# Performance work log

Measured on AMD Instinct MI355X. Metric: run time of the kernel, lower is better.

Reference implementation:

```python
import jax, jax.numpy as jnp
import numpy as np
import math

D_MODEL = 1024
NUM_HEADS = 16
HEAD_DIM = D_MODEL // NUM_HEADS
BATCH = 2
SEQ = 2048
THETA = 10000.0


def _rope_tables(seq_len, head_dim, theta=THETA):
    inv_freq = 1.0 / theta ** (jnp.arange(0, head_dim, 2, dtype=jnp.float32) / head_dim)
    pos = jnp.arange(seq_len, dtype=jnp.float32)
    freqs = jnp.outer(pos, inv_freq)                 # [S, hd/2]
    emb = jnp.concatenate([freqs, freqs], axis=-1)   # [S, hd]
    return jnp.cos(emb), jnp.sin(emb)


def _rotate_half(x):
    x1, x2 = jnp.split(x, 2, axis=-1)
    return jnp.concatenate([-x2, x1], axis=-1)


def setup_inputs() -> dict:
    key = jax.random.key(0)
    k1, k2, k3 = jax.random.split(key, 3)
    x = jax.random.normal(k1, (BATCH, SEQ, D_MODEL), dtype=jnp.float32)
    # causal mask: 1 where attend allowed, 0 where masked
    mask = jnp.tril(jnp.ones((SEQ, SEQ), dtype=jnp.int32))[None, None]
    w_qkv = jax.random.normal(k2, (D_MODEL, 3 * D_MODEL), dtype=jnp.float32) / math.sqrt(D_MODEL)
    w_out = jax.random.normal(k3, (D_MODEL, D_MODEL), dtype=jnp.float32) / math.sqrt(D_MODEL)
    return {"x": x, "mask": mask, "w_qkv": w_qkv, "w_out": w_out}


def reference(x, mask, w_qkv, w_out):
    B, S, _ = x.shape
    qkv = x @ w_qkv                                          # [B,S,3*D]
    qkv = qkv.reshape(B, S, 3, NUM_HEADS, HEAD_DIM)
    qkv = jnp.transpose(qkv, (2, 0, 3, 1, 4))                # [3,B,H,S,hd]
    q, k, v = qkv[0], qkv[1], qkv[2]
    cos, sin = _rope_tables(S, HEAD_DIM)                     # [S,hd]
    cos = cos[None, None]; sin = sin[None, None]
    q = q * cos + _rotate_half(q) * sin
    k = k * cos + _rotate_half(k) * sin
    scores = jnp.einsum('bhqd,bhkd->bhqk', q, k) / math.sqrt(HEAD_DIM)
    scores = jnp.where(mask == 0, -jnp.inf, scores)
    attn = jax.nn.softmax(scores, axis=-1)                   # dropout p=0 (eval)
    out = jnp.einsum('bhqk,bhkd->bhqd', attn, v)             # [B,H,S,hd]
    out = jnp.transpose(out, (0, 2, 1, 3)).reshape(B, S, D_MODEL)
    return out @ w_out
```

## Files before the change

kernel.cpp:

```cpp
#include <hip/hip_runtime.h>

typedef __bf16 bf16;
typedef __bf16 bf16x4 __attribute__((ext_vector_type(4)));
typedef __bf16 bf16x8 __attribute__((ext_vector_type(8)));
typedef short s16x4 __attribute__((ext_vector_type(4)));
typedef float f32x4 __attribute__((ext_vector_type(4)));

constexpr int BATCH = 2;
constexpr int SEQ   = 2048;
constexpr int DMODEL= 1024;
constexpr int NH    = 16;
constexpr int HD    = 64;
constexpr int M_ROWS= BATCH * SEQ;
constexpr int N_QKV = 3 * DMODEL;

__device__ __forceinline__ void gl_lds16(const bf16* g, bf16* l) {
  __builtin_amdgcn_global_load_lds(
      (const __attribute__((address_space(1))) unsigned int*)g,
      (__attribute__((address_space(3))) unsigned int*)l, 16, 0, 0);
}

__device__ __forceinline__ f32x4 mfma_16x16x16_bf16(bf16x4 a, bf16x4 b,
                                                    f32x4 c) {
#if defined(__HIP_DEVICE_COMPILE__)
  union { bf16x4 h; s16x4 s; } ua{a}, ub{b};
  return __builtin_amdgcn_mfma_f32_16x16x16bf16_1k(ua.s, ub.s, c, 0, 0, 0);
#else
  return c;
#endif
}

__global__ __launch_bounds__(256) void prep_kernel(
    const float* __restrict__ x, const float* __restrict__ w_qkv,
    const float* __restrict__ w_out, bf16* __restrict__ xb,
    bf16* __restrict__ WqkvT, bf16* __restrict__ WoutT) {
  const int bx = blockIdx.x, t = threadIdx.x;
  if (bx < 2048) {
    const int i = (bx * 256 + t) * 8;
    float4 f0 = *(const float4*)&x[i];
    float4 f1 = *(const float4*)&x[i + 4];
    bf16x8 v;
    v[0] = (bf16)f0.x; v[1] = (bf16)f0.y; v[2] = (bf16)f0.z; v[3] = (bf16)f0.w;
    v[4] = (bf16)f1.x; v[5] = (bf16)f1.y; v[6] = (bf16)f1.z; v[7] = (bf16)f1.w;
    *(bf16x8*)&xb[i] = v;
    return;
  }
  __shared__ float tile[32][33];
  const float* src;
  bf16* dst;
  int R, C, c0, r0;
  if (bx < 5120) {
    const int idx = bx - 2048;
    src = w_qkv; dst = WqkvT; R = DMODEL; C = N_QKV;
    c0 = (idx % 96) * 32; r0 = (idx / 96) * 32;
  } else {
    const int idx = bx - 5120;
    src = w_out; dst = WoutT; R = DMODEL; C = DMODEL;
    c0 = (idx & 31) * 32; r0 = (idx >> 5) * 32;
  }
  const int tx = t & 31, ty = t >> 5;
#pragma unroll
  for (int i = 0; i < 4; i++)
    tile[ty + 8 * i][tx] = src[(size_t)(r0 + ty + 8 * i) * C + c0 + tx];
  __syncthreads();
#pragma unroll
  for (int i = 0; i < 4; i++)
    dst[(size_t)(c0 + ty + 8 * i) * R + r0 + tx] = (bf16)tile[tx][ty + 8 * i];
}

#define GEMM_BODY(A, BT, K)                                                    \
  __shared__ bf16 smem[8448];                                                  \
  bf16* As = smem;                                                             \
  bf16* Bs = smem + 4096;                                                      \
  const int t = threadIdx.x;                                                   \
  const int m0 = blockIdx.y * 128;                                             \
  const int n0 = blockIdx.x * 128;                                             \
  const int w = t >> 6, lane = t & 63, g = lane >> 4, li = lane & 15;          \
  const int r0w = (w & 1) * 64, c0w = (w >> 1) * 64;                           \
  f32x4 acc[4][4] = {};                                                        \
  for (int k0 = 0; k0 < (K); k0 += 32) {                                       \
    __syncthreads();                                                           \
    _Pragma("unroll") for (int c = 0; c < 2; c++) {                            \
      const int idx = (w * 2 + c) * 64 + lane;                                 \
      const int row = idx >> 2, col = (idx & 3) * 8;                           \
      gl_lds16(&(A)[(size_t)(m0 + row) * (K) + k0 + col],                      \
               &As[(w * 2 + c) * 512]);                                        \
      gl_lds16(&(BT)[(size_t)(n0 + row) * (K) + k0 + col],                     \
               &Bs[(w * 2 + c) * 512]);                                        \
    }                                                                          \
    __syncthreads();                                                           \
    bf16x8 a[4], b[4];                                                         \
    _Pragma("unroll") for (int mt = 0; mt < 4; mt++)                           \
        a[mt] = *(const bf16x8*)&As[(r0w + mt * 16 + li) * 32 + g * 8];        \
    _Pragma("unroll") for (int nt = 0; nt < 4; nt++)                           \
        b[nt] = *(const bf16x8*)&Bs[(c0w + nt * 16 + li) * 32 + g * 8];        \
    _Pragma("unroll") for (int mt = 0; mt < 4; mt++)                           \
        _Pragma("unroll") for (int nt = 0; nt < 4; nt++)                       \
            acc[mt][nt] = __builtin_amdgcn_mfma_f32_16x16x32_bf16(             \
                a[mt], b[nt], acc[mt][nt], 0, 0, 0);                           \
  }

__global__ __launch_bounds__(256) void gemm_out64(
    const bf16* __restrict__ A, const bf16* __restrict__ BT,
    float* __restrict__ C, int M, int N, int K) {
  __shared__ bf16 As[64 * 32];
  __shared__ bf16 Bs[128 * 32];
  const int t = threadIdx.x;
  const int m0 = blockIdx.y * 64;
  const int n0 = blockIdx.x * 128;
  const int w = t >> 6, lane = t & 63, g = lane >> 4, li = lane & 15;
  const int r0w = (w & 1) * 32, c0w = (w >> 1) * 64;
  f32x4 acc[2][4] = {};
  for (int k0 = 0; k0 < K; k0 += 32) {
    __syncthreads();
    {
      const int idx = w * 64 + lane;
      const int row = idx >> 2, col = (idx & 3) * 8;
      gl_lds16(&A[(size_t)(m0 + row) * K + k0 + col], &As[w * 512]);
    }
#pragma unroll
    for (int c = 0; c < 2; c++) {
      const int idx = (w * 2 + c) * 64 + lane;
      const int row = idx >> 2, col = (idx & 3) * 8;
      gl_lds16(&BT[(size_t)(n0 + row) * K + k0 + col], &Bs[(w * 2 + c) * 512]);
    }
    __syncthreads();
    bf16x8 a[2], b[4];
#pragma unroll
    for (int mt = 0; mt < 2; mt++)
      a[mt] = *(const bf16x8*)&As[(r0w + mt * 16 + li) * 32 + g * 8];
#pragma unroll
    for (int nt = 0; nt < 4; nt++)
      b[nt] = *(const bf16x8*)&Bs[(c0w + nt * 16 + li) * 32 + g * 8];
#pragma unroll
    for (int mt = 0; mt < 2; mt++)
#pragma unroll
      for (int nt = 0; nt < 4; nt++)
        acc[mt][nt] = __builtin_amdgcn_mfma_f32_16x16x32_bf16(
            a[mt], b[nt], acc[mt][nt], 0, 0, 0);
  }
#pragma unroll
  for (int mt = 0; mt < 2; mt++)
#pragma unroll
    for (int nt = 0; nt < 4; nt++)
#pragma unroll
      for (int r = 0; r < 4; r++) {
        const int m = m0 + r0w + mt * 16 + g * 4 + r;
        const int n = n0 + c0w + nt * 16 + li;
        C[(size_t)m * N + n] = acc[mt][nt][r];
      }
}

__global__ __launch_bounds__(256) void gemm_qkv_rope(
    const bf16* __restrict__ A, const bf16* __restrict__ BT,
    bf16* __restrict__ Qb, bf16* __restrict__ Kb, bf16* __restrict__ Vt) {
  constexpr int K = DMODEL;
  GEMM_BODY(A, BT, K)

  const int region = n0 >> 10;
  const int b = m0 >> 11;
  const int h = ((n0 + c0w) >> 6) & 15;
  const size_t bh = (size_t)(b * NH + h);

  if (region < 2) {
    bf16* dst = region == 0 ? Qb : Kb;
    const float outsc = region == 0 ? 0.125f * 1.44269504f : 1.f;
    const float L = 13.287712379549449f;
    const float if0 = exp2f(-(float)(2 * li) / 64.f * L);
    const float if1 = exp2f(-(float)(2 * (li + 16)) / 64.f * L);
    bf16* lw = smem + w * 2112;
#pragma unroll
    for (int pass = 0; pass < 2; pass++) {
      __syncthreads();
#pragma unroll
      for (int mtl = 0; mtl < 2; mtl++) {
        const int mt = pass * 2 + mtl;
#pragma unroll
        for (int r = 0; r < 4; r++) {
          const int s = (m0 + r0w + mt * 16 + g * 4 + r) & (SEQ - 1);
          float cs[2], sn[2];
          __sincosf((float)s * if0, &sn[0], &cs[0]);
          __sincosf((float)s * if1, &sn[1], &cs[1]);
#pragma unroll
          for (int nt = 0; nt < 4; nt++) {
            const int par = nt & 1;
            const float a = acc[mt][nt][r];
            const float ap = acc[mt][nt ^ 2][r];
            const float v = (nt < 2) ? a * cs[par] - ap * sn[par]
                                     : a * cs[par] + ap * sn[par];
            lw[(mtl * 16 + g * 4 + r) * 66 + nt * 16 + li] =
                (bf16)(v * outsc);
          }
        }
      }
      __syncthreads();
      const int rowl = lane >> 1, dh = (lane & 1) * 32;
      const int s = (m0 + r0w + pass * 32 + rowl) & (SEQ - 1);
      bf16* gdst = &dst[(bh * SEQ + s) * HD + dh];
      const bf16* lsrc = &lw[rowl * 66 + dh];
#pragma unroll
      for (int c = 0; c < 4; c++)
        *(bf16x8*)&gdst[c * 8] = *(const bf16x8*)&lsrc[c * 8];
    }
  } else {
#pragma unroll
    for (int mt = 0; mt < 4; mt++)
#pragma unroll
      for (int nt = 0; nt < 4; nt++) {
        const int s = (m0 + r0w + mt * 16 + g * 4) & (SEQ - 1);
        const int d = nt * 16 + li;
        bf16x4 v;
#pragma unroll
        for (int r = 0; r < 4; r++) v[r] = (bf16)acc[mt][nt][r];
        *(bf16x4*)&Vt[(bh * HD + d) * SEQ + s] = v;
      }
  }
}

__global__ __launch_bounds__(256, 4) void flash_attn8(
    const bf16* __restrict__ Q, const bf16* __restrict__ Kb,
    const bf16* __restrict__ Vt, bf16* __restrict__ Oout) {
  const int bx = blockIdx.x;
  const int qt = 31 - (bx >> 5);
  const int bh = bx & 31;
  const int q0 = qt * 64;
  const int t = threadIdx.x, w = t >> 6, lane = t & 63, g = lane >> 4,
            li = lane & 15;

  __shared__ bf16 Ks[2][4096];
  __shared__ bf16 Vs[2][4096];

  const bf16* Qh = Q  + (size_t)bh * SEQ * HD;
  const bf16* Kh = Kb + (size_t)bh * SEQ * HD;
  const bf16* Vh = Vt + (size_t)bh * HD * SEQ;

  const int qw = q0 + w * 16;

  bf16x8 qf[2];
#pragma unroll
  for (int ks = 0; ks < 2; ks++)
    qf[ks] = *(const bf16x8*)&Qh[(size_t)(qw + li) * HD + ks * 32 + g * 8];

  f32x4 o[4] = {};
  f32x4 o4  = {};
  bf16x4 ones;
#pragma unroll
  for (int r = 0; r < 4; r++) ones[r] = (bf16)1.f;

  const int p0 = w * 128 + lane, p1 = p0 + 64;
  const int sr0 = p0 >> 3, sc0 = ((p0 & 7) ^ (sr0 & 7)) * 8;
  const int sr1 = p1 >> 3, sc1 = ((p1 & 7) ^ (sr1 & 7)) * 8;
  const int lo0 = w * 1024, lo1 = w * 1024 + 512;

  const int jend = q0 + 64;

  gl_lds16(&Kh[(size_t)sr0 * HD + sc0], &Ks[0][lo0]);
  gl_lds16(&Kh[(size_t)sr1 * HD + sc1], &Ks[0][lo1]);
  gl_lds16(&Vh[(size_t)sr0 * SEQ + sc0], &Vs[0][lo0]);
  gl_lds16(&Vh[(size_t)sr1 * SEQ + sc1], &Vs[0][lo1]);
  __syncthreads();

  for (int j0 = 0; j0 < jend; j0 += 64) {
    const int cur = (j0 >> 6) & 1, nxt = cur ^ 1;
    if (j0 + 64 < jend) {
      const int jn = j0 + 64;
      gl_lds16(&Kh[(size_t)(jn + sr0) * HD + sc0], &Ks[nxt][lo0]);
      gl_lds16(&Kh[(size_t)(jn + sr1) * HD + sc1], &Ks[nxt][lo1]);
      gl_lds16(&Vh[(size_t)sr0 * SEQ + jn + sc0], &Vs[nxt][lo0]);
      gl_lds16(&Vh[(size_t)sr1 * SEQ + jn + sc1], &Vs[nxt][lo1]);
    }

    if (j0 <= qw + 15) {
      const bool masked = (j0 + 63 > qw);
      const int ntlim = min(4, ((qw + 15 - j0) >> 4) + 1);

      f32x4 sacc[4] = {};
#pragma unroll
      for (int ks = 0; ks < 2; ks++)
#pragma unroll
        for (int nt = 0; nt < 4; nt++) {
          if (nt >= ntlim) continue;
          const int rK = nt * 16 + li;
          const int pK = rK * 8 + ((ks * 4 + g) ^ (li & 7));
          bf16x8 kf = *(const bf16x8*)&Ks[cur][pK * 8];
          sacc[nt] = __builtin_amdgcn_mfma_f32_16x16x32_bf16(kf, qf[ks],
                                                             sacc[nt], 0, 0, 0);
        }

      bf16x4 pf[4];
#pragma unroll
      for (int nt = 0; nt < 4; nt++) {
        if (nt >= ntlim) continue;
#pragma unroll
        for (int r = 0; r < 4; r++) {
          float v = sacc[nt][r];
          if (masked) {
            const int kk = j0 + nt * 16 + g * 4 + r;
            v = (kk <= qw + li) ? v : -1e30f;
          }
          pf[nt][r] = (bf16)exp2f(v);
        }
      }

#pragma unroll
      for (int nt = 0; nt < 4; nt++) {
        if (nt >= ntlim) continue;
        o4 = mfma_16x16x16_bf16(ones, pf[nt], o4);
#pragma unroll
        for (int dt = 0; dt < 4; dt++) {
          const int rV = dt * 16 + li;
          const int cg = nt * 2 + (g >> 1);
          const int pV = rV * 8 + (cg ^ (rV & 7));
          bf16x4 vfrag = *(const bf16x4*)&Vs[cur][pV * 8 + (g & 1) * 4];
          o[dt] = mfma_16x16x16_bf16(vfrag, pf[nt], o[dt]);
        }
      }
    }
    __syncthreads();
  }

  const float inv_l = 1.f / o4[0];

  const int b = bh >> 4, h = bh & 15;
  const int s = qw + li;
#pragma unroll
  for (int dt = 0; dt < 4; dt++) {
    bf16x4 ov;
#pragma unroll
    for (int r = 0; r < 4; r++) ov[r] = (bf16)(o[dt][r] * inv_l);
    *(bf16x4*)&Oout[((size_t)(b * SEQ + s)) * DMODEL + h * 64 + dt * 16 +
                    g * 4] = ov;
  }
}

extern "C" void kernel_launch(void* const* d_in, const int* in_sizes, int n_in,
                              void* d_out, int out_size, void* d_ws,
                              size_t ws_size, hipStream_t stream) {
  const float* x     = (const float*)d_in[0];
  const float* w_qkv = (const float*)d_in[2];
  const float* w_out = (const float*)d_in[3];
  float* out = (float*)d_out;

  char* ws = (char*)d_ws;
  bf16* WqkvT = (bf16*)(ws);
  bf16* WoutT = (bf16*)(ws + 6291456);
  bf16* xb    = (bf16*)(ws + 8388608);
  bf16* Qb    = (bf16*)(ws + 16777216);
  bf16* Kbuf  = (bf16*)(ws + 25165824);
  bf16* Vt    = (bf16*)(ws + 33554432);
  bf16* attn  = (bf16*)(ws + 41943040);

  prep_kernel<<<dim3(6144), 256, 0, stream>>>(x, w_qkv, w_out, xb, WqkvT,
                                              WoutT);
  gemm_qkv_rope<<<dim3(N_QKV / 128, M_ROWS / 128), 256, 0, stream>>>(
      xb, WqkvT, Qb, Kbuf, Vt);
  flash_attn8<<<dim3(1024), 256, 0, stream>>>(Qb, Kbuf, Vt, attn);
  gemm_out64<<<dim3(DMODEL / 128, M_ROWS / 64), 256, 0, stream>>>(
      attn, WoutT, out, M_ROWS, DMODEL, DMODEL);
}
```

Before: 207.0 us.

## Triple-buffer K/V tiles in flash attention with explicit vmcnt waits and priority

Switches the attention kernel's K/V shared-memory staging from double to triple buffering, so each loop iteration prefetches two tiles ahead. The full __syncthreads is replaced by explicit s_waitcnt vmcnt counts plus raw s_barrier and sched_barrier, which lets one tile's loads stay in flight across the barrier. MFMA sections are wrapped in s_setprio raises. The costs are 48KB of LDS per block and launch bounds lowered from 4 to 3 blocks per CU, which may reduce occupancy.

```diff
diff --git a/kernel.cpp b/kernel.cpp
--- a/kernel.cpp
+++ b/kernel.cpp
@@ -217,7 +217,7 @@
   }
 }
 
-__global__ __launch_bounds__(256, 4) void flash_attn8(
+__global__ __launch_bounds__(256, 3) void flash_attn9(
     const bf16* __restrict__ Q, const bf16* __restrict__ Kb,
     const bf16* __restrict__ Vt, bf16* __restrict__ Oout) {
   const int bx = blockIdx.x;
@@ -227,8 +227,8 @@
   const int t = threadIdx.x, w = t >> 6, lane = t & 63, g = lane >> 4,
             li = lane & 15;
 
-  __shared__ bf16 Ks[2][4096];
-  __shared__ bf16 Vs[2][4096];
+  __shared__ bf16 Ks[3][4096];
+  __shared__ bf16 Vs[3][4096];
 
   const bf16* Qh = Q  + (size_t)bh * SEQ * HD;
   const bf16* Kh = Kb + (size_t)bh * SEQ * HD;
@@ -240,6 +240,7 @@
 #pragma unroll
   for (int ks = 0; ks < 2; ks++)
     qf[ks] = *(const bf16x8*)&Qh[(size_t)(qw + li) * HD + ks * 32 + g * 8];
+  asm volatile("s_waitcnt vmcnt(0)" ::: "memory");
 
   f32x4 o[4] = {};
   f32x4 o4  = {};
@@ -252,29 +253,39 @@
   const int sr1 = p1 >> 3, sc1 = ((p1 & 7) ^ (sr1 & 7)) * 8;
   const int lo0 = w * 1024, lo1 = w * 1024 + 512;
 
-  const int jend = q0 + 64;
-
-  gl_lds16(&Kh[(size_t)sr0 * HD + sc0], &Ks[0][lo0]);
-  gl_lds16(&Kh[(size_t)sr1 * HD + sc1], &Ks[0][lo1]);
-  gl_lds16(&Vh[(size_t)sr0 * SEQ + sc0], &Vs[0][lo0]);
-  gl_lds16(&Vh[(size_t)sr1 * SEQ + sc1], &Vs[0][lo1]);
-  __syncthreads();
-
-  for (int j0 = 0; j0 < jend; j0 += 64) {
-    const int cur = (j0 >> 6) & 1, nxt = cur ^ 1;
-    if (j0 + 64 < jend) {
-      const int jn = j0 + 64;
-      gl_lds16(&Kh[(size_t)(jn + sr0) * HD + sc0], &Ks[nxt][lo0]);
-      gl_lds16(&Kh[(size_t)(jn + sr1) * HD + sc1], &Ks[nxt][lo1]);
-      gl_lds16(&Vh[(size_t)sr0 * SEQ + jn + sc0], &Vs[nxt][lo0]);
-      gl_lds16(&Vh[(size_t)sr1 * SEQ + jn + sc1], &Vs[nxt][lo1]);
-    }
+  const int ntiles = qt + 1;
+
+#define STAGE_T(ti, buf)                                                 \
+  {                                                                      \
+    const int jn = (ti) * 64;                                            \
+    gl_lds16(&Kh[(size_t)(jn + sr0) * HD + sc0], &Ks[buf][lo0]);         \
+    gl_lds16(&Kh[(size_t)(jn + sr1) * HD + sc1], &Ks[buf][lo1]);         \
+    gl_lds16(&Vh[(size_t)sr0 * SEQ + jn + sc0], &Vs[buf][lo0]);          \
+    gl_lds16(&Vh[(size_t)sr1 * SEQ + jn + sc1], &Vs[buf][lo1]);          \
+  }
+
+  STAGE_T(0, 0);
+  if (ntiles > 1) {
+    STAGE_T(1, 1);
+    asm volatile("s_waitcnt vmcnt(4)" ::: "memory");
+  } else {
+    asm volatile("s_waitcnt vmcnt(0)" ::: "memory");
+  }
+  __builtin_amdgcn_s_barrier();
+  __builtin_amdgcn_sched_barrier(0);
+
+  int cur = 0, stb = 2;
+  for (int ti = 0; ti < ntiles; ++ti) {
+    const int j0 = ti * 64;
+    const bool more2 = (ti + 2 < ntiles);
+    if (more2) STAGE_T(ti + 2, stb);
 
     if (j0 <= qw + 15) {
       const bool masked = (j0 + 63 > qw);
       const int ntlim = min(4, ((qw + 15 - j0) >> 4) + 1);
 
       f32x4 sacc[4] = {};
+      __builtin_amdgcn_s_setprio(1);
 #pragma unroll
       for (int ks = 0; ks < 2; ks++)
 #pragma unroll
@@ -286,6 +297,7 @@
           sacc[nt] = __builtin_amdgcn_mfma_f32_16x16x32_bf16(kf, qf[ks],
                                                              sacc[nt], 0, 0, 0);
         }
+      __builtin_amdgcn_s_setprio(0);
 
       bf16x4 pf[4];
 #pragma unroll
@@ -302,6 +314,7 @@
         }
       }
 
+      __builtin_amdgcn_s_setprio(1);
 #pragma unroll
       for (int nt = 0; nt < 4; nt++) {
         if (nt >= ntlim) continue;
@@ -315,9 +328,21 @@
           o[dt] = mfma_16x16x16_bf16(vfrag, pf[nt], o[dt]);
         }
       }
+      __builtin_amdgcn_s_setprio(0);
     }
-    __syncthreads();
-  }
+
+    __builtin_amdgcn_sched_barrier(0);
+    if (more2)
+      asm volatile("s_waitcnt vmcnt(4)" ::: "memory");
+    else
+      asm volatile("s_waitcnt vmcnt(0)" ::: "memory");
+    __builtin_amdgcn_s_barrier();
+    __builtin_amdgcn_sched_barrier(0);
+
+    cur = (cur == 2) ? 0 : cur + 1;
+    stb = (stb == 2) ? 0 : stb + 1;
+  }
+#undef STAGE_T
 
   const float inv_l = 1.f / o4[0];
 
@@ -354,7 +379,7 @@
                                               WoutT);
   gemm_qkv_rope<<<dim3(N_QKV / 128, M_ROWS / 128), 256, 0, stream>>>(
       xb, WqkvT, Qb, Kbuf, Vt);
-  flash_attn8<<<dim3(1024), 256, 0, stream>>>(Qb, Kbuf, Vt, attn);
+  flash_attn9<<<dim3(1024), 256, 0, stream>>>(Qb, Kbuf, Vt, attn);
   gemm_out64<<<dim3(DMODEL / 128, M_ROWS / 64), 256, 0, stream>>>(
       attn, WoutT, out, M_ROWS, DMODEL, DMODEL);
 }
```

Result: no change. 209.2 us (+1.1%).

## Split long causal query tiles across key chunks with atomic fp32 accumulation

Applied to the files above, without the earlier changes.

Query tiles beyond the first 512 rows are split into up to four key-range chunks of 8 tiles each. A lookup table orders the 2560 blocks so the heaviest work is scheduled first. Partial unnormalized outputs and row sums are combined with fp32 atomicAdd into a zeroed workspace, and a new attn_norm kernel divides by the sum and writes bf16. The aim is to cut the long-tail imbalance of causal attention and give the GPU more parallel work. The cost is many global atomics, an extra zeroing pass folded into prep, and one extra kernel launch.

```diff
diff --git a/kernel.cpp b/kernel.cpp
--- a/kernel.cpp
+++ b/kernel.cpp
@@ -33,7 +33,8 @@
 __global__ __launch_bounds__(256) void prep_kernel(
     const float* __restrict__ x, const float* __restrict__ w_qkv,
     const float* __restrict__ w_out, bf16* __restrict__ xb,
-    bf16* __restrict__ WqkvT, bf16* __restrict__ WoutT) {
+    bf16* __restrict__ WqkvT, bf16* __restrict__ WoutT,
+    float* __restrict__ zbase) {
   const int bx = blockIdx.x, t = threadIdx.x;
   if (bx < 2048) {
     const int i = (bx * 256 + t) * 8;
@@ -43,6 +44,13 @@
     v[0] = (bf16)f0.x; v[1] = (bf16)f0.y; v[2] = (bf16)f0.z; v[3] = (bf16)f0.w;
     v[4] = (bf16)f1.x; v[5] = (bf16)f1.y; v[6] = (bf16)f1.z; v[7] = (bf16)f1.w;
     *(bf16x8*)&xb[i] = v;
+    return;
+  }
+  if (bx >= 6144) {
+    const size_t base = ((size_t)(bx - 6144) * 256 + t) * 16;
+    const float4 z = {0.f, 0.f, 0.f, 0.f};
+#pragma unroll
+    for (int i = 0; i < 4; i++) *(float4*)&zbase[base + i * 4] = z;
     return;
   }
   __shared__ float tile[32][33];
@@ -217,13 +225,28 @@
   }
 }
 
-__global__ __launch_bounds__(256, 4) void flash_attn8(
+__device__ const unsigned char CHUNK_TAB[80] = {
+    124, 125, 126, 127,
+    120, 121, 122, 116, 117, 118, 112, 113, 114, 108, 109, 110,
+    104, 105, 106, 100, 101, 102, 96,  97,  98,  92,  93,  94,
+    88,  89,  84,  85,  80,  81,  76,  77,  72,  73,  68,  69,
+    64,  65,  60,  61,
+    56,  52,  48,  44,  40,  36,  32,  28,
+    24,  57,  90,  123, 20,  53,  86,  119, 16,  49,  82,  115,
+    12,  45,  78,  111, 8,   41,  74,  107, 4,   37,  70,  103,
+    0,   33,  66,  99};
+
+__global__ __launch_bounds__(256, 4) void flash_attn10(
     const bf16* __restrict__ Q, const bf16* __restrict__ Kb,
-    const bf16* __restrict__ Vt, bf16* __restrict__ Oout) {
+    const bf16* __restrict__ Vt, bf16* __restrict__ Oout,
+    float* __restrict__ O32, float* __restrict__ L32) {
   const int bx = blockIdx.x;
-  const int qt = 31 - (bx >> 5);
+  const unsigned char e = CHUNK_TAB[bx >> 5];
+  const int qt = e >> 2, kch = e & 3;
   const int bh = bx & 31;
   const int q0 = qt * 64;
+  const int jlo = kch * 8;
+  const int jhi = min(jlo + 8, qt + 1);
   const int t = threadIdx.x, w = t >> 6, lane = t & 63, g = lane >> 4,
             li = lane & 15;
 
@@ -252,17 +275,19 @@
   const int sr1 = p1 >> 3, sc1 = ((p1 & 7) ^ (sr1 & 7)) * 8;
   const int lo0 = w * 1024, lo1 = w * 1024 + 512;
 
-  const int jend = q0 + 64;
-
-  gl_lds16(&Kh[(size_t)sr0 * HD + sc0], &Ks[0][lo0]);
-  gl_lds16(&Kh[(size_t)sr1 * HD + sc1], &Ks[0][lo1]);
-  gl_lds16(&Vh[(size_t)sr0 * SEQ + sc0], &Vs[0][lo0]);
-  gl_lds16(&Vh[(size_t)sr1 * SEQ + sc1], &Vs[0][lo1]);
+  {
+    const int jn = jlo * 64;
+    gl_lds16(&Kh[(size_t)(jn + sr0) * HD + sc0], &Ks[jlo & 1][lo0]);
+    gl_lds16(&Kh[(size_t)(jn + sr1) * HD + sc1], &Ks[jlo & 1][lo1]);
+    gl_lds16(&Vh[(size_t)sr0 * SEQ + jn + sc0], &Vs[jlo & 1][lo0]);
+    gl_lds16(&Vh[(size_t)sr1 * SEQ + jn + sc1], &Vs[jlo & 1][lo1]);
+  }
   __syncthreads();
 
-  for (int j0 = 0; j0 < jend; j0 += 64) {
-    const int cur = (j0 >> 6) & 1, nxt = cur ^ 1;
-    if (j0 + 64 < jend) {
+  for (int ti = jlo; ti < jhi; ++ti) {
+    const int j0 = ti * 64;
+    const int cur = ti & 1, nxt = cur ^ 1;
+    if (ti + 1 < jhi) {
       const int jn = j0 + 64;
       gl_lds16(&Kh[(size_t)(jn + sr0) * HD + sc0], &Ks[nxt][lo0]);
       gl_lds16(&Kh[(size_t)(jn + sr1) * HD + sc1], &Ks[nxt][lo1]);
@@ -319,18 +344,48 @@
     __syncthreads();
   }
 
-  const float inv_l = 1.f / o4[0];
-
-  const int b = bh >> 4, h = bh & 15;
-  const int s = qw + li;
-#pragma unroll
-  for (int dt = 0; dt < 4; dt++) {
-    bf16x4 ov;
-#pragma unroll
-    for (int r = 0; r < 4; r++) ov[r] = (bf16)(o[dt][r] * inv_l);
-    *(bf16x4*)&Oout[((size_t)(b * SEQ + s)) * DMODEL + h * 64 + dt * 16 +
-                    g * 4] = ov;
-  }
+  if (qt <= 7) {
+    const float inv_l = 1.f / o4[0];
+    const int b = bh >> 4, h = bh & 15;
+    const int s = qw + li;
+#pragma unroll
+    for (int dt = 0; dt < 4; dt++) {
+      bf16x4 ov;
+#pragma unroll
+      for (int r = 0; r < 4; r++) ov[r] = (bf16)(o[dt][r] * inv_l);
+      *(bf16x4*)&Oout[((size_t)(b * SEQ + s)) * DMODEL + h * 64 + dt * 16 +
+                      g * 4] = ov;
+    }
+  } else {
+    const int srel = qw + li - 512;
+    if (g == 0) atomicAdd(&L32[bh * 1536 + srel], o4[0]);
+    float* od = &O32[((size_t)bh * 1536 + srel) * 64];
+#pragma unroll
+    for (int dt = 0; dt < 4; dt++)
+#pragma unroll
+      for (int r = 0; r < 4; r++)
+        atomicAdd(&od[dt * 16 + g * 4 + r], o[dt][r]);
+  }
+}
+
+__global__ __launch_bounds__(256) void attn_norm(
+    const float* __restrict__ O32, const float* __restrict__ L32,
+    bf16* __restrict__ attn) {
+  const int gi = blockIdx.x * 256 + threadIdx.x;
+  const int row = gi >> 3;
+  const int d0 = (gi & 7) * 8;
+  const int bh = row / 1536, srel = row - bh * 1536;
+  const int b = bh >> 4, h = bh & 15, s = srel + 512;
+  const float inv = 1.f / L32[row];
+  const float* src = &O32[(size_t)row * 64 + d0];
+  float4 f0 = *(const float4*)src;
+  float4 f1 = *(const float4*)(src + 4);
+  bf16x8 v;
+  v[0] = (bf16)(f0.x * inv); v[1] = (bf16)(f0.y * inv);
+  v[2] = (bf16)(f0.z * inv); v[3] = (bf16)(f0.w * inv);
+  v[4] = (bf16)(f1.x * inv); v[5] = (bf16)(f1.y * inv);
+  v[6] = (bf16)(f1.z * inv); v[7] = (bf16)(f1.w * inv);
+  *(bf16x8*)&attn[((size_t)(b * SEQ + s)) * DMODEL + h * 64 + d0] = v;
 }
 
 extern "C" void kernel_launch(void* const* d_in, const int* in_sizes, int n_in,
@@ -349,12 +404,15 @@
   bf16* Kbuf  = (bf16*)(ws + 25165824);
   bf16* Vt    = (bf16*)(ws + 33554432);
   bf16* attn  = (bf16*)(ws + 41943040);
-
-  prep_kernel<<<dim3(6144), 256, 0, stream>>>(x, w_qkv, w_out, xb, WqkvT,
-                                              WoutT);
+  float* O32  = (float*)(ws + 50331648);
+  float* L32  = (float*)(ws + 62914560);
+
+  prep_kernel<<<dim3(6924), 256, 0, stream>>>(x, w_qkv, w_out, xb, WqkvT,
+                                              WoutT, O32);
   gemm_qkv_rope<<<dim3(N_QKV / 128, M_ROWS / 128), 256, 0, stream>>>(
       xb, WqkvT, Qb, Kbuf, Vt);
-  flash_attn8<<<dim3(1024), 256, 0, stream>>>(Qb, Kbuf, Vt, attn);
+  flash_attn10<<<dim3(2560), 256, 0, stream>>>(Qb, Kbuf, Vt, attn, O32, L32);
+  attn_norm<<<dim3(1536), 256, 0, stream>>>(O32, L32, attn);
   gemm_out64<<<dim3(DMODEL / 128, M_ROWS / 64), 256, 0, stream>>>(
       attn, WoutT, out, M_ROWS, DMODEL, DMODEL);
 }
```

New measurement: 294.2 us. 1.42x slower.

## Split long causal query tiles across two blocks and merge the partial results

Applied to the files above, without the earlier changes.

Each query tile at index 16 or above is split into two key ranges, each handled by its own block. Those blocks write fp32 partial outputs and row sums to workspace, and a new merge kernel adds them and normalizes into the bf16 attention buffer. A lookup table orders the work so the longest pieces are scheduled first, which shortens the longest per-block chain of key tiles caused by the causal triangle. The cost is extra fp32 partial traffic and one more kernel launch.

```diff
diff --git a/kernel.cpp b/kernel.cpp
--- a/kernel.cpp
+++ b/kernel.cpp
@@ -217,13 +217,30 @@
   }
 }
 
-__global__ __launch_bounds__(256, 4) void flash_attn8(
+__device__ const unsigned char WORK_TAB[48] = {
+    125, 126, 121, 60,
+    122, 117, 118, 113, 56,
+    114, 109, 110, 105, 52,
+    106, 101, 102, 97,  48,
+    98,  93,  94,  89,  44,
+    90,  85,  86,  81,  40,
+    82,  77,  78,  73,  36,
+    74,  69,  70,  65,  32,
+    66,  28,
+    24,  20,  16,  12,  8,   4,   0};
+
+__global__ __launch_bounds__(256, 4) void flash_attn11(
     const bf16* __restrict__ Q, const bf16* __restrict__ Kb,
-    const bf16* __restrict__ Vt, bf16* __restrict__ Oout) {
+    const bf16* __restrict__ Vt, bf16* __restrict__ Oout,
+    float* __restrict__ Opart, float* __restrict__ Lpart) {
   const int bx = blockIdx.x;
-  const int qt = 31 - (bx >> 5);
+  const int e = WORK_TAB[bx >> 5];
+  const int qt = e >> 2, code = e & 3;
   const int bh = bx & 31;
   const int q0 = qt * 64;
+  const int jmid = (qt + 2) >> 1;
+  const int jlo = (code == 2) ? jmid : 0;
+  const int jhi = (code == 1) ? jmid : qt + 1;
   const int t = threadIdx.x, w = t >> 6, lane = t & 63, g = lane >> 4,
             li = lane & 15;
 
@@ -252,17 +269,19 @@
   const int sr1 = p1 >> 3, sc1 = ((p1 & 7) ^ (sr1 & 7)) * 8;
   const int lo0 = w * 1024, lo1 = w * 1024 + 512;
 
-  const int jend = q0 + 64;
-
-  gl_lds16(&Kh[(size_t)sr0 * HD + sc0], &Ks[0][lo0]);
-  gl_lds16(&Kh[(size_t)sr1 * HD + sc1], &Ks[0][lo1]);
-  gl_lds16(&Vh[(size_t)sr0 * SEQ + sc0], &Vs[0][lo0]);
-  gl_lds16(&Vh[(size_t)sr1 * SEQ + sc1], &Vs[0][lo1]);
+  {
+    const int jn = jlo * 64;
+    gl_lds16(&Kh[(size_t)(jn + sr0) * HD + sc0], &Ks[jlo & 1][lo0]);
+    gl_lds16(&Kh[(size_t)(jn + sr1) * HD + sc1], &Ks[jlo & 1][lo1]);
+    gl_lds16(&Vh[(size_t)sr0 * SEQ + jn + sc0], &Vs[jlo & 1][lo0]);
+    gl_lds16(&Vh[(size_t)sr1 * SEQ + jn + sc1], &Vs[jlo & 1][lo1]);
+  }
   __syncthreads();
 
-  for (int j0 = 0; j0 < jend; j0 += 64) {
-    const int cur = (j0 >> 6) & 1, nxt = cur ^ 1;
-    if (j0 + 64 < jend) {
+  for (int ti = jlo; ti < jhi; ++ti) {
+    const int j0 = ti * 64;
+    const int cur = ti & 1, nxt = cur ^ 1;
+    if (ti + 1 < jhi) {
       const int jn = j0 + 64;
       gl_lds16(&Kh[(size_t)(jn + sr0) * HD + sc0], &Ks[nxt][lo0]);
       gl_lds16(&Kh[(size_t)(jn + sr1) * HD + sc1], &Ks[nxt][lo1]);
@@ -319,18 +338,52 @@
     __syncthreads();
   }
 
-  const float inv_l = 1.f / o4[0];
-
-  const int b = bh >> 4, h = bh & 15;
-  const int s = qw + li;
-#pragma unroll
-  for (int dt = 0; dt < 4; dt++) {
-    bf16x4 ov;
-#pragma unroll
-    for (int r = 0; r < 4; r++) ov[r] = (bf16)(o[dt][r] * inv_l);
-    *(bf16x4*)&Oout[((size_t)(b * SEQ + s)) * DMODEL + h * 64 + dt * 16 +
-                    g * 4] = ov;
-  }
+  if (code == 0) {
+    const float inv_l = 1.f / o4[0];
+    const int b = bh >> 4, h = bh & 15;
+    const int s = qw + li;
+#pragma unroll
+    for (int dt = 0; dt < 4; dt++) {
+      bf16x4 ov;
+#pragma unroll
+      for (int r = 0; r < 4; r++) ov[r] = (bf16)(o[dt][r] * inv_l);
+      *(bf16x4*)&Oout[((size_t)(b * SEQ + s)) * DMODEL + h * 64 + dt * 16 +
+                      g * 4] = ov;
+    }
+  } else {
+    const int srel = qw + li - 1024;
+    const size_t slot = ((size_t)(bh * 2 + (code - 1)) * 1024 + srel);
+    if (g == 0) Lpart[slot] = o4[0];
+    float* od = &Opart[slot * 64];
+#pragma unroll
+    for (int dt = 0; dt < 4; dt++)
+      *(f32x4*)&od[dt * 16 + g * 4] = o[dt];
+  }
+}
+
+__global__ __launch_bounds__(256) void attn_merge(
+    const float* __restrict__ Opart, const float* __restrict__ Lpart,
+    bf16* __restrict__ attn) {
+  const int gi = blockIdx.x * 256 + threadIdx.x;
+  const int row = gi >> 3;
+  const int d0 = (gi & 7) * 8;
+  const int bh = row >> 10, srel = row & 1023;
+  const int b = bh >> 4, h = bh & 15, s = srel + 1024;
+  const size_t s0 = ((size_t)(bh * 2) * 1024 + srel);
+  const size_t s1 = s0 + 1024;
+  const float inv = 1.f / (Lpart[s0] + Lpart[s1]);
+  const float* p0 = &Opart[s0 * 64 + d0];
+  const float* p1 = &Opart[s1 * 64 + d0];
+  float4 a0 = *(const float4*)p0;
+  float4 a1 = *(const float4*)(p0 + 4);
+  float4 b0 = *(const float4*)p1;
+  float4 b1 = *(const float4*)(p1 + 4);
+  bf16x8 v;
+  v[0] = (bf16)((a0.x + b0.x) * inv); v[1] = (bf16)((a0.y + b0.y) * inv);
+  v[2] = (bf16)((a0.z + b0.z) * inv); v[3] = (bf16)((a0.w + b0.w) * inv);
+  v[4] = (bf16)((a1.x + b1.x) * inv); v[5] = (bf16)((a1.y + b1.y) * inv);
+  v[6] = (bf16)((a1.z + b1.z) * inv); v[7] = (bf16)((a1.w + b1.w) * inv);
+  *(bf16x8*)&attn[((size_t)(b * SEQ + s)) * DMODEL + h * 64 + d0] = v;
 }
 
 extern "C" void kernel_launch(void* const* d_in, const int* in_sizes, int n_in,
@@ -349,12 +402,16 @@
   bf16* Kbuf  = (bf16*)(ws + 25165824);
   bf16* Vt    = (bf16*)(ws + 33554432);
   bf16* attn  = (bf16*)(ws + 41943040);
+  float* Opart= (float*)(ws + 50331648);
+  float* Lpart= (float*)(ws + 67108864);
 
   prep_kernel<<<dim3(6144), 256, 0, stream>>>(x, w_qkv, w_out, xb, WqkvT,
                                               WoutT);
   gemm_qkv_rope<<<dim3(N_QKV / 128, M_ROWS / 128), 256, 0, stream>>>(
       xb, WqkvT, Qb, Kbuf, Vt);
-  flash_attn8<<<dim3(1024), 256, 0, stream>>>(Qb, Kbuf, Vt, attn);
+  flash_attn11<<<dim3(1536), 256, 0, stream>>>(Qb, Kbuf, Vt, attn, Opart,
+                                               Lpart);
+  attn_merge<<<dim3(1024), 256, 0, stream>>>(Opart, Lpart, attn);
   gemm_out64<<<dim3(DMODEL / 128, M_ROWS / 64), 256, 0, stream>>>(
       attn, WoutT, out, M_ROWS, DMODEL, DMODEL);
 }
```

New measurement: 202.6 us. 2.1% less time.
